# Kernel tuning notes

Hardware: AMD Instinct MI355X
Metric: run time of the kernel (lower is better)

The kernel has to match this reference:

```python
import jax, jax.numpy as jnp
import numpy as np

H, W = 2048, 2048
N_PTS = 1_000_000
N_POS = 100_000
EMB = 32

def setup_inputs() -> dict:
    key = jax.random.key(0)
    ks = jax.random.split(key, 12)
    scale = jnp.array([H, W], dtype=jnp.float32)
    x = jax.random.uniform(ks[0], (N_PTS, 2), dtype=jnp.float32) * (scale - 1.0)
    positions = jax.random.uniform(ks[1], (N_POS, 2), dtype=jnp.float32) * scale
    neighbor_map = jax.random.randint(ks[2], (H, W, 4), 0, N_POS, dtype=jnp.int32)
    embeddings = jax.random.normal(ks[3], (N_POS, EMB), dtype=jnp.float32) * 0.001
    W1 = jax.random.normal(ks[4], (64, EMB), dtype=jnp.float32) / np.sqrt(EMB)
    b1 = jax.random.normal(ks[5], (64,), dtype=jnp.float32) * 0.01
    W2 = jax.random.normal(ks[6], (64, 64), dtype=jnp.float32) / np.sqrt(64)
    b2 = jax.random.normal(ks[7], (64,), dtype=jnp.float32) * 0.01
    W3 = jax.random.normal(ks[8], (3, 64), dtype=jnp.float32) / np.sqrt(64)
    b3 = jax.random.normal(ks[9], (3,), dtype=jnp.float32) * 0.01
    mu = jax.random.uniform(ks[10], (3,), dtype=jnp.float32)
    std = jax.random.uniform(ks[11], (3,), dtype=jnp.float32) + 0.1
    return {"x": x, "positions": positions, "neighbor_map": neighbor_map,
            "embeddings": embeddings, "W1": W1, "b1": b1, "W2": W2, "b2": b2,
            "W3": W3, "b3": b3, "mu": mu, "std": std}

def reference(x, positions, neighbor_map, embeddings, W1, b1, W2, b2, W3, b3, mu, std):
    # LatentMap: floor -> neighbor gather -> distance-weighted embedding sum
    int_pos = jnp.floor(x).astype(jnp.int32)                 # [N, 2]
    nb = neighbor_map[int_pos[:, 0], int_pos[:, 1]]          # [N, 4]
    nb_pos = positions[nb]                                   # [N, 4, 2]
    diff = nb_pos - int_pos[:, None, :].astype(jnp.float32)  # [N, 4, 2]
    dist = jax.lax.stop_gradient(jnp.linalg.norm(diff, axis=-1))  # [N, 4]
    latent = jnp.einsum('nk,nkd->nd', dist, embeddings[nb])  # [N, 32]
    # tiny MLP (equinox Linear: y = x @ W.T + b), relu on hidden layers
    h = jax.nn.relu(latent @ W1.T + b1)
    h = jax.nn.relu(h @ W2.T + b2)
    out = h @ W3.T + b3                                      # [N, 3]
    # denormalize (mu/std are stop_gradient'ed in the original)
    out = out * jax.lax.stop_gradient(std) + jax.lax.stop_gradient(mu)
    # NaN-guarded clip: per-point cond(any NaN -> mu, else clip to [0,1])
    has_nan = jnp.any(jnp.isnan(out), axis=-1, keepdims=True)
    return jnp.where(has_nan, jax.lax.stop_gradient(mu), jnp.clip(out, 0.0, 1.0))
```

## Files before the change

### kernel.cpp

```cpp
#include <hip/hip_runtime.h>
#include <hip/hip_bf16.h>


typedef __attribute__((ext_vector_type(2))) float f32x2;
typedef __attribute__((ext_vector_type(4))) float f32x4;
typedef __attribute__((ext_vector_type(4))) int   i32x4;
typedef __attribute__((ext_vector_type(8))) short s16x8;

#define GRID_W  2048
#define LSTR    36
#define LOOFF   16
#define PSTR    68
#define W2OFF   (4 * 32 * LSTR)
#define W1OFF   (W2OFF + 2048)
#define SEL_HI  0x05040100u
#define SEL_LO  0x07060302u
#define LGKM0   0xC07F

static __device__ __forceinline__ unsigned bits_bf2(__hip_bfloat162 h) {
    union { __hip_bfloat162 b; unsigned u; } cv; cv.b = h; return cv.u;
}
static __device__ __forceinline__ void split2_packed(float v0, float v1, unsigned &p0, unsigned &p1) {
    float2 f; f.x = v0; f.y = v1;
    unsigned hu = bits_bf2(__float22bfloat162_rn(f));
    float2 d;
    d.x = v0 - __uint_as_float(hu << 16);
    d.y = v1 - __uint_as_float(hu & 0xffff0000u);
    unsigned lu = bits_bf2(__float22bfloat162_rn(d));
    p0 = (hu & 0xffffu) | (lu << 16);
    p1 = (hu >> 16) | (lu & 0xffff0000u);
}
static __device__ __forceinline__ void split2_frag(float v0, float v1, unsigned &hu, unsigned &lu) {
    float2 f; f.x = v0; f.y = v1;
    hu = bits_bf2(__float22bfloat162_rn(f));
    float2 d;
    d.x = v0 - __uint_as_float(hu << 16);
    d.y = v1 - __uint_as_float(hu & 0xffff0000u);
    lu = bits_bf2(__float22bfloat162_rn(d));
}
static __device__ __forceinline__ s16x8 unpack8(uint4 q0, uint4 q1, unsigned sel) {
    union { unsigned u[4]; s16x8 v; } r;
    r.u[0] = __builtin_amdgcn_perm(q0.y, q0.x, sel);
    r.u[1] = __builtin_amdgcn_perm(q0.w, q0.z, sel);
    r.u[2] = __builtin_amdgcn_perm(q1.y, q1.x, sel);
    r.u[3] = __builtin_amdgcn_perm(q1.w, q1.z, sel);
    return r.v;
}
static __device__ __forceinline__ s16x8 load_wbf(const float* p) {
    f32x4 a = ((const f32x4*)p)[0];
    f32x4 b = ((const f32x4*)p)[1];
    union { unsigned u[4]; s16x8 v; } r;
    float2 f;
    f.x = a.x; f.y = a.y; r.u[0] = bits_bf2(__float22bfloat162_rn(f));
    f.x = a.z; f.y = a.w; r.u[1] = bits_bf2(__float22bfloat162_rn(f));
    f.x = b.x; f.y = b.y; r.u[2] = bits_bf2(__float22bfloat162_rn(f));
    f.x = b.z; f.y = b.w; r.u[3] = bits_bf2(__float22bfloat162_rn(f));
    return r.v;
}
static __device__ __forceinline__ void lds_fence() {
    __builtin_amdgcn_wave_barrier();
    __builtin_amdgcn_s_waitcnt(LGKM0);
    __builtin_amdgcn_wave_barrier();
}
template <int OFFS>
static __device__ __forceinline__ float swz_bcast(float v) {
    return __uint_as_float((unsigned)__builtin_amdgcn_ds_swizzle(
        (int)__float_as_uint(v), OFFS));
}

__global__ __launch_bounds__(256, 5) void fused_persistent(
    const float* __restrict__ x,
    const float* __restrict__ positions,
    const int*   __restrict__ nbmap,
    const float* __restrict__ emb,
    const float* __restrict__ W1,
    const float* __restrict__ b1,
    const float* __restrict__ W2,
    const float* __restrict__ b2,
    const float* __restrict__ W3,
    const float* __restrict__ b3,
    const float* __restrict__ mu,
    const float* __restrict__ sd,
    float* __restrict__ out,
    int npts)
{
    const int tid  = threadIdx.x;
    const int w    = tid >> 6;
    const int lid  = tid & 63;
    const int quad = lid >> 4;
    const int m16  = lid & 15;
    const int c8   = lid & 7;
    const int pr   = lid >> 3;
    const int ksel = c8 & 3;

    const int nwav = gridDim.x * 4;
    const int wgid = blockIdx.x * 4 + w;
    const int NCH  = (npts + 31) >> 5;

    __shared__ __align__(16) unsigned lat_lds[W1OFF + 1024];
    unsigned* latw = lat_lds + w * 32 * LSTR;
    unsigned* hb   = latw;
    unsigned* w2b  = lat_lds + W2OFF;
    unsigned* w1b  = lat_lds + W1OFF;

    if (w == 0) {
#pragma unroll
        for (int s = 0; s < 2; ++s)
#pragma unroll
            for (int nt = 0; nt < 4; ++nt) {
                union { s16x8 v; uint4 q; } cv;
                cv.v = load_wbf(W2 + (nt * 16 + m16) * 64 + s * 32 + quad * 8);
                *(uint4*)(w2b + ((s * 4 + nt) * 64 + lid) * 4) = cv.q;
            }
#pragma unroll
        for (int nt = 0; nt < 4; ++nt) {
            union { s16x8 v; uint4 q; } cv;
            cv.v = load_wbf(W1 + (nt * 16 + m16) * 32 + quad * 8);
            *(uint4*)(w1b + (nt * 64 + lid) * 4) = cv.q;
        }
    }
    __syncthreads();
    if (wgid >= NCH) return;

    const f32x2* Xv  = (const f32x2*)x;
    const f32x2* Pv  = (const f32x2*)positions;
    const i32x4* NBq = (const i32x4*)nbmap;

    s16x8 w3f[2];
#pragma unroll
    for (int s = 0; s < 2; ++s) {
        if (m16 < 3) {
            w3f[s] = load_wbf(W3 + m16 * 64 + s * 32 + quad * 8);
        } else {
            s16x8 z = {0, 0, 0, 0, 0, 0, 0, 0};
            w3f[s] = z;
        }
    }
    float b1v[4], b2v[4];
#pragma unroll
    for (int nt = 0; nt < 4; ++nt) { b1v[nt] = b1[nt * 16 + m16]; b2v[nt] = b2[nt * 16 + m16]; }
    const int mm = (m16 < 3) ? m16 : 0;
    const float b3m = b3[mm], sdm = sd[mm], mum = mu[mm];

    f32x2 xv[4], xvn[4];
    i32x4 nb[4], nbn[4];
#pragma unroll
    for (int p = 0; p < 4; ++p) {
        int g = wgid * 32 + p * 8 + pr;
        g = (g < npts) ? g : (npts - 1);
        xv[p] = Xv[g];
    }
#pragma unroll
    for (int p = 0; p < 4; ++p) {
        int i0 = (int)xv[p].x, i1 = (int)xv[p].y;
        nb[p] = NBq[i0 * GRID_W + i1];
    }

    for (int c = wgid; c < NCH; c += nwav) {
        const int cn = c + nwav;
        const bool hn = (cn < NCH);

        if (hn) {
#pragma unroll
            for (int p = 0; p < 4; ++p) {
                int g = cn * 32 + p * 8 + pr;
                g = (g < npts) ? g : (npts - 1);
                xvn[p] = Xv[g];
            }
        }

#pragma unroll
        for (int p = 0; p < 4; ++p) {
            f32x2 xvp = xv[p];
            float f0 = (float)(int)xvp.x, f1 = (float)(int)xvp.y;
            i32x4 n4 = nb[p];
            int ids[4] = {n4.x, n4.y, n4.z, n4.w};
            int id_sel = ids[0];
            id_sel = (ksel == 1) ? ids[1] : id_sel;
            id_sel = (ksel == 2) ? ids[2] : id_sel;
            id_sel = (ksel == 3) ? ids[3] : id_sel;
            f32x2 pp = Pv[id_sel];
            float dx = pp.x - f0, dy = pp.y - f1;
            float dsel = sqrtf(dx * dx + dy * dy);
            float dd[4];
            dd[0] = swz_bcast<0x18>(dsel);
            dd[1] = swz_bcast<0x38>(dsel);
            dd[2] = swz_bcast<0x58>(dsel);
            dd[3] = swz_bcast<0x78>(dsel);
            float a0 = 0.f, a1 = 0.f, a2 = 0.f, a3 = 0.f;
#pragma unroll
            for (int k = 0; k < 4; ++k) {
                f32x4 e = *(const f32x4*)(emb + ids[k] * 32 + c8 * 4);
                a0 = fmaf(dd[k], e.x, a0); a1 = fmaf(dd[k], e.y, a1);
                a2 = fmaf(dd[k], e.z, a2); a3 = fmaf(dd[k], e.w, a3);
            }
            unsigned h0, l0, h1, l1;
            split2_frag(a0, a1, h0, l0);
            split2_frag(a2, a3, h1, l1);
            unsigned* rowp = latw + (p * 8 + pr) * LSTR;
            uint2 hv; hv.x = h0; hv.y = h1;
            uint2 lv; lv.x = l0; lv.y = l1;
            *(uint2*)(rowp + c8 * 2)         = hv;
            *(uint2*)(rowp + LOOFF + c8 * 2) = lv;
        }
        lds_fence();

        s16x8 AH[2], AL[2];
#pragma unroll
        for (int t = 0; t < 2; ++t) {
            const unsigned* rowp = latw + (t * 16 + m16) * LSTR;
            union { uint4 q; s16x8 v; } ch, cl;
            ch.q = *(const uint4*)(rowp + quad * 4);
            cl.q = *(const uint4*)(rowp + LOOFF + quad * 4);
            AH[t] = ch.v;
            AL[t] = cl.v;
        }
        lds_fence();

        if (hn) {
#pragma unroll
            for (int p = 0; p < 4; ++p) {
                int i0 = (int)xvn[p].x, i1 = (int)xvn[p].y;
                nbn[p] = NBq[i0 * GRID_W + i1];
            }
        }

#pragma unroll
        for (int t = 0; t < 2; ++t) {
            s16x8 ah = AH[t], al = AL[t];
            f32x4 c1[4];
#pragma unroll
            for (int nt = 0; nt < 4; ++nt) {
                union { uint4 q; s16x8 v; } wc;
                wc.q = *(const uint4*)(w1b + (nt * 64 + lid) * 4);
                f32x4 cc = {0.f, 0.f, 0.f, 0.f};
                cc = __builtin_amdgcn_mfma_f32_16x16x32_bf16(al, wc.v, cc, 0, 0, 0);
                cc = __builtin_amdgcn_mfma_f32_16x16x32_bf16(ah, wc.v, cc, 0, 0, 0);
                c1[nt] = cc;
            }
            __builtin_amdgcn_wave_barrier();
#pragma unroll
            for (int nt = 0; nt < 4; ++nt)
#pragma unroll
                for (int r = 0; r < 4; r += 2) {
                    float v0 = fmaxf(c1[nt][r]     + b1v[nt], 0.f);
                    float v1 = fmaxf(c1[nt][r + 1] + b1v[nt], 0.f);
                    unsigned p0, p1; split2_packed(v0, v1, p0, p1);
                    hb[(quad * 4 + r)     * PSTR + nt * 16 + m16] = p0;
                    hb[(quad * 4 + r + 1) * PSTR + nt * 16 + m16] = p1;
                }
            lds_fence();

            f32x4 c2[4] = {{0.f,0.f,0.f,0.f},{0.f,0.f,0.f,0.f},{0.f,0.f,0.f,0.f},{0.f,0.f,0.f,0.f}};
#pragma unroll
            for (int s = 0; s < 2; ++s) {
                const unsigned* rp = hb + m16 * PSTR + s * 32 + quad * 8;
                uint4 h0 = *(const uint4*)rp;
                uint4 h1 = *(const uint4*)(rp + 4);
                s16x8 a2h = unpack8(h0, h1, SEL_HI);
                s16x8 a2l = unpack8(h0, h1, SEL_LO);
#pragma unroll
                for (int nt = 0; nt < 4; ++nt) {
                    union { uint4 q; s16x8 v; } wc;
                    wc.q = *(const uint4*)(w2b + ((s * 4 + nt) * 64 + lid) * 4);
                    c2[nt] = __builtin_amdgcn_mfma_f32_16x16x32_bf16(a2l, wc.v, c2[nt], 0, 0, 0);
                    c2[nt] = __builtin_amdgcn_mfma_f32_16x16x32_bf16(a2h, wc.v, c2[nt], 0, 0, 0);
                }
            }
            lds_fence();
#pragma unroll
            for (int nt = 0; nt < 4; ++nt)
#pragma unroll
                for (int r = 0; r < 4; r += 2) {
                    float v0 = fmaxf(c2[nt][r]     + b2v[nt], 0.f);
                    float v1 = fmaxf(c2[nt][r + 1] + b2v[nt], 0.f);
                    unsigned p0, p1; split2_packed(v0, v1, p0, p1);
                    hb[(quad * 4 + r)     * PSTR + nt * 16 + m16] = p0;
                    hb[(quad * 4 + r + 1) * PSTR + nt * 16 + m16] = p1;
                }
            lds_fence();

            f32x4 c3 = {0.f, 0.f, 0.f, 0.f};
#pragma unroll
            for (int s = 0; s < 2; ++s) {
                const unsigned* rp = hb + m16 * PSTR + s * 32 + quad * 8;
                uint4 h0 = *(const uint4*)rp;
                uint4 h1 = *(const uint4*)(rp + 4);
                s16x8 a3h = unpack8(h0, h1, SEL_HI);
                s16x8 a3l = unpack8(h0, h1, SEL_LO);
                c3 = __builtin_amdgcn_mfma_f32_16x16x32_bf16(a3l, w3f[s], c3, 0, 0, 0);
                c3 = __builtin_amdgcn_mfma_f32_16x16x32_bf16(a3h, w3f[s], c3, 0, 0, 0);
            }
            lds_fence();
#pragma unroll
            for (int r = 0; r < 4; ++r) {
                float v = (c3[r] + b3m) * sdm + mum;
                v = fminf(fmaxf(v, 0.f), 1.f);
                int gpt = c * 32 + t * 16 + quad * 4 + r;
                if (m16 < 3 && gpt < npts) out[(size_t)gpt * 3 + m16] = v;
            }
        }

        if (hn) {
#pragma unroll
            for (int p = 0; p < 4; ++p) { xv[p] = xvn[p]; nb[p] = nbn[p]; }
        }
    }
}

extern "C" void kernel_launch(void* const* d_in, const int* in_sizes, int n_in,
                              void* d_out, int out_size, void* d_ws, size_t ws_size,
                              hipStream_t stream) {
    const float* x         = (const float*)d_in[0];
    const float* positions = (const float*)d_in[1];
    const int*   nbmap     = (const int*)d_in[2];
    const float* emb       = (const float*)d_in[3];
    const float* W1        = (const float*)d_in[4];
    const float* b1        = (const float*)d_in[5];
    const float* W2        = (const float*)d_in[6];
    const float* b2        = (const float*)d_in[7];
    const float* W3        = (const float*)d_in[8];
    const float* b3        = (const float*)d_in[9];
    const float* mu        = (const float*)d_in[10];
    const float* sd        = (const float*)d_in[11];
    float* out = (float*)d_out;

    int npts = in_sizes[0] / 2;
    int nch = (npts + 31) / 32;
    int blocks = 1280;
    int maxb = (nch + 3) / 4;
    if (blocks > maxb) blocks = maxb;
    fused_persistent<<<blocks, 256, 0, stream>>>(x, positions, nbmap, emb,
                                                 W1, b1, W2, b2, W3, b3, mu, sd,
                                                 out, npts);
}
```

Before: 209.5 us.

## Add atomic work-stealing for tail chunks in persistent kernel

The persistent kernel keeps its static round-robin chunk assignment only for the evenly divisible part of the work. Each wave then claims the leftover chunks through a global atomic counter kept in workspace, which is zeroed by a memset before launch. The goal is to balance the tail so that waves finishing early pick up the remaining chunks. In exchange it adds an extra memset call, one atomic per wave per stolen chunk, and less prefetch overlap on the stolen chunks.

```diff
diff --git a/kernel.cpp b/kernel.cpp
--- a/kernel.cpp
+++ b/kernel.cpp
@@ -68,6 +68,7 @@
         (int)__float_as_uint(v), OFFS));
 }
 
+template <bool STEAL>
 __global__ __launch_bounds__(256, 5) void fused_persistent(
     const float* __restrict__ x,
     const float* __restrict__ positions,
@@ -82,6 +83,8 @@
     const float* __restrict__ mu,
     const float* __restrict__ sd,
     float* __restrict__ out,
+    int*   __restrict__ ctr,
+    int    SEND,
     int npts)
 {
     const int tid  = threadIdx.x;
@@ -142,11 +145,12 @@
     const int mm = (m16 < 3) ? m16 : 0;
     const float b3m = b3[mm], sdm = sd[mm], mum = mu[mm];
 
+    int c = wgid;
     f32x2 xv[4], xvn[4];
     i32x4 nb[4], nbn[4];
 #pragma unroll
     for (int p = 0; p < 4; ++p) {
-        int g = wgid * 32 + p * 8 + pr;
+        int g = c * 32 + p * 8 + pr;
         g = (g < npts) ? g : (npts - 1);
         xv[p] = Xv[g];
     }
@@ -156,17 +160,20 @@
         nb[p] = NBq[i0 * GRID_W + i1];
     }
 
-    for (int c = wgid; c < NCH; c += nwav) {
-        const int cn = c + nwav;
-        const bool hn = (cn < NCH);
-
-        if (hn) {
+    for (;;) {
+        const bool nstatic = (c + nwav < SEND);
+        int cn = -1;
+        int pend = 0;
+        if (nstatic) {
+            cn = c + nwav;
 #pragma unroll
             for (int p = 0; p < 4; ++p) {
                 int g = cn * 32 + p * 8 + pr;
                 g = (g < npts) ? g : (npts - 1);
                 xvn[p] = Xv[g];
             }
+        } else if (STEAL) {
+            if (lid == 0) pend = atomicAdd(ctr, 1);
         }
 
 #pragma unroll
@@ -203,6 +210,21 @@
             *(uint2*)(rowp + c8 * 2)         = hv;
             *(uint2*)(rowp + LOOFF + c8 * 2) = lv;
         }
+
+        if (STEAL && !nstatic) {
+            int ticket = __builtin_amdgcn_readlane(pend, 0);
+            cn = SEND + ticket;
+            if (cn >= NCH) cn = -1;
+            if (cn >= 0) {
+#pragma unroll
+                for (int p = 0; p < 4; ++p) {
+                    int g = cn * 32 + p * 8 + pr;
+                    g = (g < npts) ? g : (npts - 1);
+                    xvn[p] = Xv[g];
+                }
+            }
+        }
+        const bool hn = (cn >= 0);
         lds_fence();
 
         s16x8 AH[2], AL[2];
@@ -301,10 +323,10 @@
             }
         }
 
-        if (hn) {
-#pragma unroll
-            for (int p = 0; p < 4; ++p) { xv[p] = xvn[p]; nb[p] = nbn[p]; }
-        }
+        if (!hn) break;
+#pragma unroll
+        for (int p = 0; p < 4; ++p) { xv[p] = xvn[p]; nb[p] = nbn[p]; }
+        c = cn;
     }
 }
 
@@ -330,7 +352,17 @@
     int blocks = 1280;
     int maxb = (nch + 3) / 4;
     if (blocks > maxb) blocks = maxb;
-    fused_persistent<<<blocks, 256, 0, stream>>>(x, positions, nbmap, emb,
-                                                 W1, b1, W2, b2, W3, b3, mu, sd,
-                                                 out, npts);
-}
+    int nwav = blocks * 4;
+
+    if (d_ws != nullptr && ws_size >= 16 && nch >= nwav) {
+        int send = (nch / nwav) * nwav;
+        hipMemsetAsync(d_ws, 0, 16, stream);
+        fused_persistent<true><<<blocks, 256, 0, stream>>>(
+            x, positions, nbmap, emb, W1, b1, W2, b2, W3, b3, mu, sd,
+            out, (int*)d_ws, send, npts);
+    } else {
+        fused_persistent<false><<<blocks, 256, 0, stream>>>(
+            x, positions, nbmap, emb, W1, b1, W2, b2, W3, b3, mu, sd,
+            out, nullptr, nch, npts);
+    }
+}
```

Result: slower. 248.4 us (+18.6%).
